# Optimization experiments

Measured on AMD Instinct MI355X. Metric: run time of the kernel, lower is better.

Reference implementation:

```python
import jax, jax.numpy as jnp
import numpy as np

HIDDEN = 2048
NUM_HEADS = 8
NUM_KV_HEADS = 1
HEAD_DIM = 256
ROPE_THETA = 10000.0
B, S = 2, 2048


def setup_inputs() -> dict:
    key = jax.random.key(0)
    k1, k2, k3, k4, k5 = jax.random.split(key, 5)
    scale = 0.02
    hidden_states = jax.random.normal(k1, (B, S, HIDDEN), dtype=jnp.float32)
    Wq = jax.random.normal(k2, (HIDDEN, NUM_HEADS * HEAD_DIM), dtype=jnp.float32) * scale
    Wk = jax.random.normal(k3, (HIDDEN, NUM_KV_HEADS * HEAD_DIM), dtype=jnp.float32) * scale
    Wv = jax.random.normal(k4, (HIDDEN, NUM_KV_HEADS * HEAD_DIM), dtype=jnp.float32) * scale
    Wo = jax.random.normal(k5, (NUM_HEADS * HEAD_DIM, HIDDEN), dtype=jnp.float32) * scale
    # causal mask: 1 = attend, 0 = masked (module adds -1e9 where mask==0)
    attention_mask = jnp.tril(jnp.ones((S, S), dtype=jnp.int32))[None, None].repeat(B, axis=0)
    position_ids = jnp.arange(S, dtype=jnp.int32)[None, :].repeat(B, axis=0)
    return {"hidden_states": hidden_states, "Wq": Wq, "Wk": Wk, "Wv": Wv,
            "Wo": Wo, "attention_mask": attention_mask, "position_ids": position_ids}


def _rotate_half(x):
    half = x.shape[-1] // 2
    return jnp.concatenate([-x[..., half:], x[..., :half]], axis=-1)


def _rope_cos_sin(position_ids, head_dim, theta):
    inv_freq = 1.0 / (theta ** (jnp.arange(0, head_dim, 2, dtype=jnp.float32) / head_dim))
    freqs = position_ids.astype(jnp.float32)[:, :, None] * inv_freq[None, None, :]  # [B,S,D/2]
    emb = jnp.concatenate([freqs, freqs], axis=-1)  # [B,S,D]
    return jnp.cos(emb)[:, None], jnp.sin(emb)[:, None]  # [B,1,S,D]


def reference(hidden_states, Wq, Wk, Wv, Wo, attention_mask, position_ids):
    bsz, q_len, _ = hidden_states.shape
    q = (hidden_states @ Wq).reshape(bsz, q_len, NUM_HEADS, HEAD_DIM).transpose(0, 2, 1, 3)
    k = (hidden_states @ Wk).reshape(bsz, q_len, NUM_KV_HEADS, HEAD_DIM).transpose(0, 2, 1, 3)
    v = (hidden_states @ Wv).reshape(bsz, q_len, NUM_KV_HEADS, HEAD_DIM).transpose(0, 2, 1, 3)
    q = q / jnp.sqrt(jnp.float32(HEAD_DIM))  # scale before RoPE, as in source
    cos, sin = _rope_cos_sin(position_ids, HEAD_DIM, ROPE_THETA)
    q = q * cos + _rotate_half(q) * sin
    k = k * cos + _rotate_half(k) * sin
    # GQA: repeat kv heads (prefill: cache == current k,v)
    groups = NUM_HEADS // NUM_KV_HEADS
    k = jnp.repeat(k, groups, axis=1)
    v = jnp.repeat(v, groups, axis=1)
    attn = jnp.einsum('bhqd,bhkd->bhqk', q, k)  # [B,H,S,S]
    additive = jnp.where(attention_mask == 0, jnp.float32(-1e9), jnp.float32(0.0))
    attn = jax.nn.softmax(attn + additive, axis=-1)
    out = jnp.einsum('bhqk,bhkd->bhqd', attn, v)
    out = out.transpose(0, 2, 1, 3).reshape(bsz, q_len, NUM_HEADS * HEAD_DIM)
    out = out @ Wo
    return out, attn
```

## Files before the change

kernel.cpp:

```cpp
#include <hip/hip_runtime.h>

typedef __bf16 bf16_t;
typedef __attribute__((ext_vector_type(4))) float f32x4;
typedef __attribute__((ext_vector_type(8))) __bf16 bf16x8;
typedef __attribute__((ext_vector_type(4))) __bf16 bf16x4;

#define DEVI __device__ __forceinline__

static constexpr int kBsz = 2, kS = 2048, kH = 8, kD = 256, kHid = 2048, kNqkv = 2560;

DEVI void gload_lds16(const void* g, void* l) {
  __builtin_amdgcn_global_load_lds(
      (__attribute__((address_space(1))) unsigned int*)g,
      (__attribute__((address_space(3))) unsigned int*)l, 16, 0, 0);
}

__global__ __launch_bounds__(256) void prep_all(
    const float* __restrict__ hs, const float* __restrict__ Wq,
    const float* __restrict__ Wk, const float* __restrict__ Wv,
    const float* __restrict__ Wo, bf16_t* __restrict__ hsb,
    bf16_t* __restrict__ WqkvT, bf16_t* __restrict__ WoT,
    float* __restrict__ rowsum) {
  __shared__ float tile[32][33];
  const int zb = blockIdx.x;
  const int t = threadIdx.x;
  if (zb < 8192) {
    int idx = zb * 256 + t;
    const float4 f = ((const float4*)hs)[idx];
    bf16x4 o;
    o[0] = (bf16_t)f.x; o[1] = (bf16_t)f.y; o[2] = (bf16_t)f.z; o[3] = (bf16_t)f.w;
    ((bf16x4*)hsb)[idx] = o;
    return;
  }
  if (zb >= 17408) {
    rowsum[(zb - 17408) * 256 + t] = 0.f;
    return;
  }
  const int u = zb - 8192;
  const float* src;
  bf16_t* dst;
  int C, bx, by;
  if (u < 4096) {
    src = Wq; dst = WqkvT; C = 2048; bx = u & 63; by = u >> 6;
  } else if (u < 4608) {
    int v = u - 4096; src = Wk; dst = WqkvT + (size_t)2048 * 2048; C = 256; bx = v & 7; by = v >> 3;
  } else if (u < 5120) {
    int v = u - 4608; src = Wv; dst = WqkvT + (size_t)2304 * 2048; C = 256; bx = v & 7; by = v >> 3;
  } else {
    int v = u - 5120; src = Wo; dst = WoT; C = 2048; bx = v & 63; by = v >> 6;
  }
  int c0 = bx * 32, r0 = by * 32;
  int tx = t & 31, ty = t >> 5;
#pragma unroll
  for (int k = 0; k < 4; k++)
    tile[ty + 8 * k][tx] = src[(size_t)(r0 + ty + 8 * k) * C + c0 + tx];
  __syncthreads();
#pragma unroll
  for (int k = 0; k < 4; k++)
    dst[(size_t)(c0 + ty + 8 * k) * 2048 + r0 + tx] = (bf16_t)tile[tx][ty + 8 * k];
}

__global__ __launch_bounds__(256) void rope_tv(const bf16_t* __restrict__ qkv,
                                               const int* __restrict__ pos_ids,
                                               bf16_t* __restrict__ q_bh,
                                               bf16_t* __restrict__ k_b,
                                               bf16_t* __restrict__ vT) {
  __shared__ float tile[32][33];
  const int bid = blockIdx.x;
  const int t = threadIdx.x;
  if (bid < 16384) {
    int idx = bid * 256 + t;
    int j = idx & 127, s = (idx >> 7) & 2047, h = (idx >> 18) & 7, b = idx >> 21;
    float invf = exp2f(-0.103810253f * (float)j);
    float ang = (float)pos_ids[b * kS + s] * invf;
    float c, sn;
    sincosf(ang, &sn, &c);
    const bf16_t* src = qkv + ((size_t)(b * kS + s)) * kNqkv + h * kD;
    float x0 = (float)src[j] * 0.0625f;
    float x1 = (float)src[j + 128] * 0.0625f;
    bf16_t* dst = q_bh + ((size_t)((b * kH + h) * kS + s)) * kD;
    dst[j] = (bf16_t)(x0 * c - x1 * sn);
    dst[j + 128] = (bf16_t)(x1 * c + x0 * sn);
  } else if (bid < 18432) {
    int idx = (bid - 16384) * 256 + t;
    int j = idx & 127, s = (idx >> 7) & 2047, b = idx >> 18;
    float invf = exp2f(-0.103810253f * (float)j);
    float ang = (float)pos_ids[b * kS + s] * invf;
    float c, sn;
    sincosf(ang, &sn, &c);
    const bf16_t* src = qkv + ((size_t)(b * kS + s)) * kNqkv + 2048;
    float x0 = (float)src[j];
    float x1 = (float)src[j + 128];
    bf16_t* dst = k_b + ((size_t)(b * kS + s)) * kD;
    dst[j] = (bf16_t)(x0 * c - x1 * sn);
    dst[j + 128] = (bf16_t)(x1 * c + x0 * sn);
  } else {
    int u = bid - 18432;
    int d0 = (u & 7) * 32, s0 = ((u >> 3) & 63) * 32, b = u >> 9;
    int tx = t & 31, ty = t >> 5;
    const bf16_t* in = qkv + ((size_t)(b * kS + s0)) * kNqkv + 2304 + d0;
#pragma unroll
    for (int k = 0; k < 4; k++)
      tile[ty + 8 * k][tx] = (float)in[(size_t)(ty + 8 * k) * kNqkv + tx];
    __syncthreads();
    bf16_t* out = vT + ((size_t)(b * kD + d0)) * kS + s0;
#pragma unroll
    for (int k = 0; k < 4; k++)
      out[(size_t)(ty + 8 * k) * kS + tx] = (bf16_t)tile[tx][ty + 8 * k];
  }
}

__global__ __launch_bounds__(256, 4) void qk_exp(
    const bf16_t* __restrict__ q_bh, const bf16_t* __restrict__ k_b,
    bf16_t* __restrict__ P, float* __restrict__ rowsum) {
  __shared__ bf16_t ks[64 * 256];
  const int u = blockIdx.x;
  const int z = blockIdx.y;
  const int b = z >> 3;
  int rt = (int)((sqrtf(8.f * (float)u + 1.f) - 1.f) * 0.5f);
  while ((rt + 1) * (rt + 2) / 2 <= u) rt++;
  while (rt * (rt + 1) / 2 > u) rt--;
  const int kt = u - rt * (rt + 1) / 2;
  const int m0 = rt * 64, n0 = kt * 64;
  const int t = threadIdx.x, lane = t & 63, wv = t >> 6;
  const int wm2 = (wv & 1) * 32, wn2 = (wv >> 1) * 32;
  const int lrow = lane & 15, quad = lane >> 4;

  const bf16_t* kb = k_b + (size_t)b * kS * kD;
#pragma unroll
  for (int i = 0; i < 8; i++) {
    int slot = i * 256 + t;
    int r = slot >> 5;
    int c = (slot & 31) ^ (r & 7);
    gload_lds16(kb + (size_t)(n0 + r) * kD + c * 8, ks + slot * 8);
  }
  bf16x8 qf[2][8];
  {
    const bf16_t* qb = q_bh + ((size_t)z * kS + m0) * kD;
#pragma unroll
    for (int mi = 0; mi < 2; mi++)
#pragma unroll
      for (int k8 = 0; k8 < 8; k8++)
        qf[mi][k8] = *(const bf16x8*)(qb + (size_t)(wm2 + mi * 16 + lrow) * kD + k8 * 32 + quad * 8);
  }
  __syncthreads();

  f32x4 acc[2][2];
#pragma unroll
  for (int mi = 0; mi < 2; mi++)
#pragma unroll
    for (int ni = 0; ni < 2; ni++) acc[mi][ni] = f32x4{0.f, 0.f, 0.f, 0.f};
  __builtin_amdgcn_s_setprio(1);
#pragma unroll
  for (int k8 = 0; k8 < 8; k8++) {
    bf16x8 bfv[2];
#pragma unroll
    for (int ni = 0; ni < 2; ni++) {
      int R = wn2 + ni * 16 + lrow;
      int c16 = (k8 * 4 + quad) ^ (R & 7);
      bfv[ni] = *(const bf16x8*)(ks + R * 256 + c16 * 8);
    }
#pragma unroll
    for (int mi = 0; mi < 2; mi++)
#pragma unroll
      for (int ni = 0; ni < 2; ni++)
        acc[mi][ni] = __builtin_amdgcn_mfma_f32_16x16x32_bf16(qf[mi][k8], bfv[ni], acc[mi][ni], 0, 0, 0);
  }
  __builtin_amdgcn_s_setprio(0);

  const bool diag = (kt == rt);
  bf16_t* pt = P + ((size_t)z * kS + m0) * kS + n0;
#pragma unroll
  for (int mi = 0; mi < 2; mi++)
#pragma unroll
    for (int rr = 0; rr < 4; rr++) {
      int ml = wm2 + mi * 16 + quad * 4 + rr;
      int mg = m0 + ml;
      float s4 = 0.f;
#pragma unroll
      for (int ni = 0; ni < 2; ni++) {
        int nl = wn2 + ni * 16 + lrow;
        int ng = n0 + nl;
        float e = __expf(fminf(acc[mi][ni][rr], 80.f));
        bool ok = !diag || ng <= mg;
        bf16_t pb = ok ? (bf16_t)e : (bf16_t)0.f;
        pt[(size_t)ml * kS + nl] = pb;
        s4 += (float)pb;
      }
      s4 += __shfl_xor(s4, 1); s4 += __shfl_xor(s4, 2);
      s4 += __shfl_xor(s4, 4); s4 += __shfl_xor(s4, 8);
      if (lrow == 0) atomicAdd(rowsum + (size_t)z * kS + mg, s4);
    }

  if (diag && !(rt & 1)) {
    bf16x8 zz = {(bf16_t)0.f, (bf16_t)0.f, (bf16_t)0.f, (bf16_t)0.f,
                 (bf16_t)0.f, (bf16_t)0.f, (bf16_t)0.f, (bf16_t)0.f};
    int r = t >> 2, cc = (t & 3) * 16;
    bf16_t* pz = P + ((size_t)z * kS + m0 + r) * kS + n0 + 64 + cc;
    *(bf16x8*)pz = zz;
    *(bf16x8*)(pz + 8) = zz;
  }
}

__global__ __launch_bounds__(256) void attn_expand(
    const bf16_t* __restrict__ P, const float* __restrict__ rowsum,
    float* __restrict__ attn) {
  const int rt = blockIdx.y, z = blockIdx.z;
  const int m0 = rt * 64;
  const int t = threadIdx.x;
  const int r = t >> 2;
  const int cbase = blockIdx.x * 512 + (t & 3) * 8;
  const int ncaus = (rt + 1) * 64;
  const float inv = 1.f / rowsum[(size_t)z * kS + m0 + r];
  const size_t rowoff = ((size_t)z * kS + m0 + r) * kS;
  const bf16_t* pr = P + rowoff;
  float* ar = attn + rowoff;
#pragma unroll
  for (int it = 0; it < 16; it++) {
    int col = cbase + it * 32;
    float4 o0, o1;
    if (col < ncaus) {
      bf16x8 pv = *(const bf16x8*)(pr + col);
      o0 = make_float4((float)pv[0] * inv, (float)pv[1] * inv,
                       (float)pv[2] * inv, (float)pv[3] * inv);
      o1 = make_float4((float)pv[4] * inv, (float)pv[5] * inv,
                       (float)pv[6] * inv, (float)pv[7] * inv);
    } else {
      o0 = make_float4(0.f, 0.f, 0.f, 0.f);
      o1 = o0;
    }
    *(float4*)(ar + col) = o0;
    *(float4*)(ar + col + 4) = o1;
  }
}

template <int OUT, int CKTR, int BAL = 0>
__global__ __launch_bounds__(256) void gemm_bt(
    const bf16_t* __restrict__ Av, const bf16_t* __restrict__ Btv, void* __restrict__ Cv,
    int K, int lda, int ldb, int ldc,
    long long aBatch, long long bBatch, int bzShift, long long cBatch,
    const float* __restrict__ rowsum) {
  constexpr int BM = 128, BN = 128, BK = 64;
  __shared__ bf16_t smem[BM * BK + BN * BK];
  bf16_t* As = smem;
  bf16_t* Bs = smem + BM * BK;
  const int z = blockIdx.z;
  const int n0 = blockIdx.x * BN;
  int byi = blockIdx.y;
  if (BAL) {
    if ((blockIdx.x ^ (blockIdx.z >> 3)) & 1) byi = gridDim.y - 1 - byi;
  }
  const int m0 = byi * BM;
  const bf16_t* Bt = Btv + (size_t)(z >> bzShift) * bBatch + (size_t)n0 * ldb;
  const int kEnd = CKTR ? ((m0 + BM < K) ? (m0 + BM) : K) : K;
  const int t = threadIdx.x;
  const int lane = t & 63, wv = t >> 6;
  const int wm = (wv & 1) << 6, wn = (wv >> 1) << 6;
  const int lrow = lane & 15, quad = lane >> 4;
  f32x4 zero = {0.f, 0.f, 0.f, 0.f};
  f32x4 acc[4][4];
#pragma unroll
  for (int i = 0; i < 4; i++)
#pragma unroll
    for (int j = 0; j < 4; j++) acc[i][j] = zero;

  const bf16_t* Ab = Av + (size_t)z * aBatch + (size_t)m0 * lda;

  for (int k0 = 0; k0 < kEnd; k0 += BK) {
    __syncthreads();
#pragma unroll
    for (int i = 0; i < 4; i++) {
      int slot = i * 256 + t;
      int r = slot >> 3, c = slot & 7;
      gload_lds16(Ab + (size_t)r * lda + k0 + c * 8, As + slot * 8);
    }
#pragma unroll
    for (int i = 0; i < 4; i++) {
      int slot = i * 256 + t;
      int r = slot >> 3, c = slot & 7;
      gload_lds16(Bt + (size_t)r * ldb + k0 + c * 8, Bs + slot * 8);
    }
    __syncthreads();
#pragma unroll
    for (int k8 = 0; k8 < 2; k8++) {
      bf16x8 af[4], bfv[4];
#pragma unroll
      for (int i = 0; i < 4; i++)
        af[i] = *(const bf16x8*)(As + (wm + i * 16 + lrow) * BK + k8 * 32 + quad * 8);
#pragma unroll
      for (int i = 0; i < 4; i++)
        bfv[i] = *(const bf16x8*)(Bs + (wn + i * 16 + lrow) * BK + k8 * 32 + quad * 8);
#pragma unroll
      for (int mi = 0; mi < 4; mi++)
#pragma unroll
        for (int ni = 0; ni < 4; ni++)
          acc[mi][ni] = __builtin_amdgcn_mfma_f32_16x16x32_bf16(af[mi], bfv[ni], acc[mi][ni], 0, 0, 0);
    }
  }

  if (OUT == 0) {
    float* C = (float*)Cv + (size_t)z * cBatch;
#pragma unroll
    for (int mi = 0; mi < 4; mi++) {
      int m = m0 + wm + mi * 16 + quad * 4;
#pragma unroll
      for (int ni = 0; ni < 4; ni++) {
        int n = n0 + wn + ni * 16 + lrow;
#pragma unroll
        for (int r = 0; r < 4; r++) C[(size_t)(m + r) * ldc + n] = acc[mi][ni][r];
      }
    }
  } else {
    __syncthreads();
#pragma unroll
    for (int mi = 0; mi < 4; mi++) {
      int mrow = wm + mi * 16 + quad * 4;
      float inv[4];
      if (OUT == 1) {
#pragma unroll
        for (int r = 0; r < 4; r++)
          inv[r] = 1.f / rowsum[(size_t)z * kS + m0 + mrow + r];
      }
#pragma unroll
      for (int ni = 0; ni < 4; ni++) {
        int ncol = wn + ni * 16 + lrow;
#pragma unroll
        for (int r = 0; r < 4; r++) {
          int m_l = mrow + r;
          int n_sw = ncol ^ ((m_l & 15) << 3);
          float v = acc[mi][ni][r];
          if (OUT == 1) v *= inv[r];
          smem[m_l * BN + n_sw] = (bf16_t)v;
        }
      }
    }
    __syncthreads();
    bf16_t* Cb = (OUT == 1)
        ? (bf16_t*)Cv + (size_t)(z >> 3) * cBatch + (size_t)(z & 7) * kD
        : (bf16_t*)Cv + (size_t)z * cBatch;
    int row = t >> 1, half = t & 1;
#pragma unroll
    for (int j = 0; j < 8; j++) {
      int c0 = half * 64 + j * 8;
      int c_sw = c0 ^ ((row & 15) << 3);
      bf16x8 v = *(const bf16x8*)(smem + row * BN + c_sw);
      *(bf16x8*)(Cb + (size_t)(m0 + row) * ldc + n0 + c0) = v;
    }
  }
}

extern "C" void kernel_launch(void* const* d_in, const int* in_sizes, int n_in,
                              void* d_out, int out_size, void* d_ws, size_t ws_size,
                              hipStream_t stream) {
  const float* hs = (const float*)d_in[0];
  const float* Wq = (const float*)d_in[1];
  const float* Wk = (const float*)d_in[2];
  const float* Wv = (const float*)d_in[3];
  const float* Wo = (const float*)d_in[4];
  const int* pos = (const int*)d_in[6];

  float* out = (float*)d_out;
  float* attn = out + (size_t)kBsz * kS * kHid;

  char* w = (char*)d_ws;
  bf16_t* hsb = (bf16_t*)w;   w += (size_t)4096 * 2048 * 2;
  bf16_t* WqkvT = (bf16_t*)w; w += (size_t)2560 * 2048 * 2;
  bf16_t* WoT = (bf16_t*)w;   w += (size_t)2048 * 2048 * 2;
  bf16_t* qkv = (bf16_t*)w;   w += (size_t)4096 * 2560 * 2;
  bf16_t* q_bh = (bf16_t*)w;  w += (size_t)8388608 * 2;
  bf16_t* k_b = (bf16_t*)w;   w += (size_t)1048576 * 2;
  bf16_t* vT = (bf16_t*)w;    w += (size_t)1048576 * 2;
  bf16_t* av = (bf16_t*)w;    w += (size_t)8388608 * 2;
  bf16_t* Pb = (bf16_t*)w;    w += (size_t)16 * 2048 * 2048 * 2;
  float* rowsum = (float*)w;  w += (size_t)16 * 2048 * 4;

  prep_all<<<17536, 256, 0, stream>>>(hs, Wq, Wk, Wv, Wo, hsb, WqkvT, WoT, rowsum);

  gemm_bt<2, 0><<<dim3(20, 32, 1), 256, 0, stream>>>(
      hsb, WqkvT, qkv, 2048, 2048, 2048, 2560, 0, 0, 0, 0, nullptr);

  rope_tv<<<19456, 256, 0, stream>>>(qkv, pos, q_bh, k_b, vT);

  qk_exp<<<dim3(528, 16), 256, 0, stream>>>(q_bh, k_b, Pb, rowsum);

  attn_expand<<<dim3(4, 32, 16), 256, 0, stream>>>(Pb, rowsum, attn);

  gemm_bt<1, 1, 1><<<dim3(2, 16, 16), 256, 0, stream>>>(
      Pb, vT, av, 2048, 2048, 2048, 2048,
      (long long)4194304, (long long)524288, 3, (long long)(kS * kHid), rowsum);

  gemm_bt<0, 0><<<dim3(16, 32, 1), 256, 0, stream>>>(
      av, WoT, out, 2048, 2048, 2048, 2048, 0, 0, 0, 0, nullptr);
}
```

Measured before the change: 739.2 us.

## Reuse K tile across two query row tiles and halve GEMM K-step

```diff
diff --git a/kernel.cpp b/kernel.cpp
--- a/kernel.cpp
+++ b/kernel.cpp
@@ -117,11 +117,11 @@
   const int u = blockIdx.x;
   const int z = blockIdx.y;
   const int b = z >> 3;
-  int rt = (int)((sqrtf(8.f * (float)u + 1.f) - 1.f) * 0.5f);
-  while ((rt + 1) * (rt + 2) / 2 <= u) rt++;
-  while (rt * (rt + 1) / 2 > u) rt--;
-  const int kt = u - rt * (rt + 1) / 2;
-  const int m0 = rt * 64, n0 = kt * 64;
+  int rtp = (int)((sqrtf(4.f * (float)u + 1.f) - 1.f) * 0.5f);
+  while ((rtp + 1) * (rtp + 2) <= u) rtp++;
+  while (rtp * (rtp + 1) > u) rtp--;
+  const int kt = u - rtp * (rtp + 1);
+  const int m0 = rtp * 128, n0 = kt * 64;
   const int t = threadIdx.x, lane = t & 63, wv = t >> 6;
   const int wm2 = (wv & 1) * 32, wn2 = (wv >> 1) * 32;
   const int lrow = lane & 15, quad = lane >> 4;
@@ -134,71 +134,68 @@
     int c = (slot & 31) ^ (r & 7);
     gload_lds16(kb + (size_t)(n0 + r) * kD + c * 8, ks + slot * 8);
   }
+  const bf16_t* qb = q_bh + ((size_t)z * kS + m0) * kD;
   bf16x8 qf[2][8];
-  {
-    const bf16_t* qb = q_bh + ((size_t)z * kS + m0) * kD;
+#pragma unroll
+  for (int mi = 0; mi < 2; mi++)
+#pragma unroll
+    for (int k8 = 0; k8 < 8; k8++)
+      qf[mi][k8] = *(const bf16x8*)(qb + (size_t)(wm2 + mi * 16 + lrow) * kD + k8 * 32 + quad * 8);
+  __syncthreads();
+
+#pragma unroll
+  for (int h = 0; h < 2; h++) {
+    if (h) {
+#pragma unroll
+      for (int mi = 0; mi < 2; mi++)
+#pragma unroll
+        for (int k8 = 0; k8 < 8; k8++)
+          qf[mi][k8] = *(const bf16x8*)(qb + (size_t)(64 + wm2 + mi * 16 + lrow) * kD + k8 * 32 + quad * 8);
+    }
+    f32x4 acc[2][2];
 #pragma unroll
     for (int mi = 0; mi < 2; mi++)
 #pragma unroll
-      for (int k8 = 0; k8 < 8; k8++)
-        qf[mi][k8] = *(const bf16x8*)(qb + (size_t)(wm2 + mi * 16 + lrow) * kD + k8 * 32 + quad * 8);
-  }
-  __syncthreads();
-
-  f32x4 acc[2][2];
-#pragma unroll
-  for (int mi = 0; mi < 2; mi++)
-#pragma unroll
-    for (int ni = 0; ni < 2; ni++) acc[mi][ni] = f32x4{0.f, 0.f, 0.f, 0.f};
-  __builtin_amdgcn_s_setprio(1);
-#pragma unroll
-  for (int k8 = 0; k8 < 8; k8++) {
-    bf16x8 bfv[2];
-#pragma unroll
-    for (int ni = 0; ni < 2; ni++) {
-      int R = wn2 + ni * 16 + lrow;
-      int c16 = (k8 * 4 + quad) ^ (R & 7);
-      bfv[ni] = *(const bf16x8*)(ks + R * 256 + c16 * 8);
-    }
+      for (int ni = 0; ni < 2; ni++) acc[mi][ni] = f32x4{0.f, 0.f, 0.f, 0.f};
+    __builtin_amdgcn_s_setprio(1);
+#pragma unroll
+    for (int k8 = 0; k8 < 8; k8++) {
+      bf16x8 bfv[2];
+#pragma unroll
+      for (int ni = 0; ni < 2; ni++) {
+        int R = wn2 + ni * 16 + lrow;
+        int c16 = (k8 * 4 + quad) ^ (R & 7);
+        bfv[ni] = *(const bf16x8*)(ks + R * 256 + c16 * 8);
+      }
+#pragma unroll
+      for (int mi = 0; mi < 2; mi++)
+#pragma unroll
+        for (int ni = 0; ni < 2; ni++)
+          acc[mi][ni] = __builtin_amdgcn_mfma_f32_16x16x32_bf16(qf[mi][k8], bfv[ni], acc[mi][ni], 0, 0, 0);
+    }
+    __builtin_amdgcn_s_setprio(0);
+
+    bf16_t* pt = P + ((size_t)z * kS + m0 + h * 64) * kS + n0;
 #pragma unroll
     for (int mi = 0; mi < 2; mi++)
 #pragma unroll
-      for (int ni = 0; ni < 2; ni++)
-        acc[mi][ni] = __builtin_amdgcn_mfma_f32_16x16x32_bf16(qf[mi][k8], bfv[ni], acc[mi][ni], 0, 0, 0);
-  }
-  __builtin_amdgcn_s_setprio(0);
-
-  const bool diag = (kt == rt);
-  bf16_t* pt = P + ((size_t)z * kS + m0) * kS + n0;
-#pragma unroll
-  for (int mi = 0; mi < 2; mi++)
-#pragma unroll
-    for (int rr = 0; rr < 4; rr++) {
-      int ml = wm2 + mi * 16 + quad * 4 + rr;
-      int mg = m0 + ml;
-      float s4 = 0.f;
-#pragma unroll
-      for (int ni = 0; ni < 2; ni++) {
-        int nl = wn2 + ni * 16 + lrow;
-        int ng = n0 + nl;
-        float e = __expf(fminf(acc[mi][ni][rr], 80.f));
-        bool ok = !diag || ng <= mg;
-        bf16_t pb = ok ? (bf16_t)e : (bf16_t)0.f;
-        pt[(size_t)ml * kS + nl] = pb;
-        s4 += (float)pb;
-      }
-      s4 += __shfl_xor(s4, 1); s4 += __shfl_xor(s4, 2);
-      s4 += __shfl_xor(s4, 4); s4 += __shfl_xor(s4, 8);
-      if (lrow == 0) atomicAdd(rowsum + (size_t)z * kS + mg, s4);
-    }
-
-  if (diag && !(rt & 1)) {
-    bf16x8 zz = {(bf16_t)0.f, (bf16_t)0.f, (bf16_t)0.f, (bf16_t)0.f,
-                 (bf16_t)0.f, (bf16_t)0.f, (bf16_t)0.f, (bf16_t)0.f};
-    int r = t >> 2, cc = (t & 3) * 16;
-    bf16_t* pz = P + ((size_t)z * kS + m0 + r) * kS + n0 + 64 + cc;
-    *(bf16x8*)pz = zz;
-    *(bf16x8*)(pz + 8) = zz;
+      for (int rr = 0; rr < 4; rr++) {
+        int lm = wm2 + mi * 16 + quad * 4 + rr;
+        int mg = m0 + h * 64 + lm;
+        float s4 = 0.f;
+#pragma unroll
+        for (int ni = 0; ni < 2; ni++) {
+          int nl = wn2 + ni * 16 + lrow;
+          int ng = n0 + nl;
+          float e = __expf(fminf(acc[mi][ni][rr], 80.f));
+          bf16_t pb = (ng <= mg) ? (bf16_t)e : (bf16_t)0.f;
+          pt[(size_t)lm * kS + nl] = pb;
+          s4 += (float)pb;
+        }
+        s4 += __shfl_xor(s4, 1); s4 += __shfl_xor(s4, 2);
+        s4 += __shfl_xor(s4, 4); s4 += __shfl_xor(s4, 8);
+        if (lrow == 0) atomicAdd(rowsum + (size_t)z * kS + mg, s4);
+      }
   }
 }
 
@@ -240,8 +237,9 @@
     int K, int lda, int ldb, int ldc,
     long long aBatch, long long bBatch, int bzShift, long long cBatch,
     const float* __restrict__ rowsum) {
-  constexpr int BM = 128, BN = 128, BK = 64;
-  __shared__ bf16_t smem[BM * BK + BN * BK];
+  constexpr int BM = 128, BN = 128, BK = 32;
+  constexpr int SME = (OUT == 0) ? (BM * BK + BN * BK) : (BM * BN);
+  __shared__ bf16_t smem[SME];
   bf16_t* As = smem;
   bf16_t* Bs = smem + BM * BK;
   const int z = blockIdx.z;
@@ -268,34 +266,29 @@
 
   for (int k0 = 0; k0 < kEnd; k0 += BK) {
     __syncthreads();
-#pragma unroll
-    for (int i = 0; i < 4; i++) {
-      int slot = i * 256 + t;
-      int r = slot >> 3, c = slot & 7;
-      gload_lds16(Ab + (size_t)r * lda + k0 + c * 8, As + slot * 8);
-    }
-#pragma unroll
-    for (int i = 0; i < 4; i++) {
-      int slot = i * 256 + t;
-      int r = slot >> 3, c = slot & 7;
-      gload_lds16(Bt + (size_t)r * ldb + k0 + c * 8, Bs + slot * 8);
-    }
-    __syncthreads();
-#pragma unroll
-    for (int k8 = 0; k8 < 2; k8++) {
-      bf16x8 af[4], bfv[4];
-#pragma unroll
-      for (int i = 0; i < 4; i++)
-        af[i] = *(const bf16x8*)(As + (wm + i * 16 + lrow) * BK + k8 * 32 + quad * 8);
-#pragma unroll
-      for (int i = 0; i < 4; i++)
-        bfv[i] = *(const bf16x8*)(Bs + (wn + i * 16 + lrow) * BK + k8 * 32 + quad * 8);
-#pragma unroll
-      for (int mi = 0; mi < 4; mi++)
-#pragma unroll
-        for (int ni = 0; ni < 4; ni++)
-          acc[mi][ni] = __builtin_amdgcn_mfma_f32_16x16x32_bf16(af[mi], bfv[ni], acc[mi][ni], 0, 0, 0);
-    }
+    {
+      const bf16_t* ga = Ab + (size_t)(t >> 2) * lda + k0 + (t & 3) * 8;
+      gload_lds16(ga, As + t * 8);
+      gload_lds16(ga + (size_t)64 * lda, As + 2048 + t * 8);
+    }
+    {
+      const bf16_t* gb = Bt + (size_t)(t >> 2) * ldb + k0 + (t & 3) * 8;
+      gload_lds16(gb, Bs + t * 8);
+      gload_lds16(gb + (size_t)64 * ldb, Bs + 2048 + t * 8);
+    }
+    __syncthreads();
+    bf16x8 af[4], bfv[4];
+#pragma unroll
+    for (int i = 0; i < 4; i++)
+      af[i] = *(const bf16x8*)(As + (wm + i * 16 + lrow) * BK + quad * 8);
+#pragma unroll
+    for (int i = 0; i < 4; i++)
+      bfv[i] = *(const bf16x8*)(Bs + (wn + i * 16 + lrow) * BK + quad * 8);
+#pragma unroll
+    for (int mi = 0; mi < 4; mi++)
+#pragma unroll
+      for (int ni = 0; ni < 4; ni++)
+        acc[mi][ni] = __builtin_amdgcn_mfma_f32_16x16x32_bf16(af[mi], bfv[ni], acc[mi][ni], 0, 0, 0);
   }
 
   if (OUT == 0) {
@@ -381,7 +374,7 @@
 
   rope_tv<<<19456, 256, 0, stream>>>(qkv, pos, q_bh, k_b, vT);
 
-  qk_exp<<<dim3(528, 16), 256, 0, stream>>>(q_bh, k_b, Pb, rowsum);
+  qk_exp<<<dim3(272, 16), 256, 0, stream>>>(q_bh, k_b, Pb, rowsum);
 
   attn_expand<<<dim3(4, 32, 16), 256, 0, stream>>>(Pb, rowsum, attn);
 
```

Result: faster. 721.4 us (-2.4%).
